# Performance work log

Measured on AMD Instinct MI355X. Metric: run time of the kernel, lower is better.

## Reference

```python
import jax, jax.numpy as jnp
from jax import lax
import numpy as np

B, T, N, F_IN, H, E, K = 8, 32, 500, 64, 128, 8000, 3
LN_EPS = 1e-5


def setup_inputs() -> dict:
    key = jax.random.key(0)
    ks = jax.random.split(key, 10)
    x = jax.random.normal(ks[0], (B, T, N, F_IN), dtype=jnp.float32)
    edge_index = jax.random.randint(ks[1], (2, E), 0, N, dtype=jnp.int64)
    edge_weight = jax.random.uniform(ks[2], (E,), dtype=jnp.float32)
    # GCNConv: linear (in->out) + bias
    W_gcn = jax.random.normal(ks[3], (F_IN, H), dtype=jnp.float32) / np.sqrt(F_IN)
    b_gcn = jnp.zeros((H,), dtype=jnp.float32)
    # Conv1d(H, H, K): weight (O, I, K)
    W_temp = jax.random.normal(ks[4], (H, H, K), dtype=jnp.float32) / np.sqrt(H * K)
    b_temp = jnp.zeros((H,), dtype=jnp.float32)
    # LayerNorm(H)
    ln_w = jnp.ones((H,), dtype=jnp.float32)
    ln_b = jnp.zeros((H,), dtype=jnp.float32)
    # residual Linear (in->out)
    W_res = jax.random.normal(ks[5], (F_IN, H), dtype=jnp.float32) / np.sqrt(F_IN)
    b_res = jnp.zeros((H,), dtype=jnp.float32)
    return {"x": x, "edge_index": edge_index, "edge_weight": edge_weight,
            "W_gcn": W_gcn, "b_gcn": b_gcn, "W_temp": W_temp, "b_temp": b_temp,
            "ln_w": ln_w, "ln_b": ln_b, "W_res": W_res, "b_res": b_res}


def reference(x, edge_index, edge_weight, W_gcn, b_gcn, W_temp, b_temp, ln_w, ln_b, W_res, b_res):
    Bv, Tv, Nv, Fv = x.shape
    Hv = W_gcn.shape[1]
    res = x @ W_res + b_res  # (B,T,N,H)

    # ---- spatial GCNConv on B*T replicated graphs (vectorized, no index offsetting) ----
    xf = x.reshape(Bv * Tv, Nv, Fv) @ W_gcn  # (BT,N,H)
    src, dst = edge_index[0], edge_index[1]
    loops = jnp.arange(Nv, dtype=edge_index.dtype)
    src2 = jnp.concatenate([src, loops])
    dst2 = jnp.concatenate([dst, loops])
    ew2 = jnp.concatenate([edge_weight, jnp.ones((Nv,), dtype=edge_weight.dtype)])
    deg = jax.ops.segment_sum(ew2, dst2, num_segments=Nv)
    dinv = jnp.where(deg > 0, deg ** -0.5, 0.0)
    norm = dinv[src2] * ew2 * dinv[dst2]  # (E+N,)
    msgs = xf[:, src2, :] * norm[None, :, None]  # (BT, E+N, H)
    agg = jax.vmap(lambda m: jax.ops.segment_sum(m, dst2, num_segments=Nv))(msgs)
    h = jax.nn.gelu(agg + b_gcn, approximate=False)  # (BT,N,H)

    # ---- temporal Conv1d over T ----
    h = h.reshape(Bv, Tv, Nv, Hv).transpose(0, 2, 3, 1).reshape(Bv * Nv, Hv, Tv)
    pad = K // 2
    h = lax.conv_general_dilated(h, W_temp, window_strides=(1,), padding=[(pad, pad)],
                                 dimension_numbers=("NCH", "OIH", "NCH"))
    h = jax.nn.gelu(h + b_temp[None, :, None], approximate=False)
    h = h.reshape(Bv, Nv, Hv, Tv).transpose(0, 3, 1, 2)  # (B,T,N,H)

    # ---- fused residual + LayerNorm over last dim ----
    y = h + res
    mu = jnp.mean(y, axis=-1, keepdims=True)
    var = jnp.mean((y - mu) ** 2, axis=-1, keepdims=True)
    return (y - mu) * lax.rsqrt(var + LN_EPS) * ln_w + ln_b
```

## Files before the change

kernel.cpp:

```cpp
#include <hip/hip_runtime.h>
#include <hip/hip_bf16.h>
#include <math.h>

#define Bv 8
#define Tv 32
#define Nv 500
#define Fin 64
#define Hv 128
#define Ev 8000
#define Kv 3
#define BT (Bv*Tv)
#define ROWS (BT*Nv)
#define TP (Tv+2)
#define KK (Kv*Hv)
#define LDSROW 136

typedef __attribute__((ext_vector_type(8))) short s8v;
typedef __attribute__((ext_vector_type(4))) float f4v;

__device__ __forceinline__ float gelu_exact(float v){
    return 0.5f*v*(1.0f + erff(v*0.70710678118654752440f));
}
__device__ __forceinline__ short f2bs(float f){
    union { __hip_bfloat16 h; short s; } u;
    u.h = __float2bfloat16(f);
    return u.s;
}
__device__ __forceinline__ float b2f(short s){
    union { unsigned int i; float f; } u;
    u.i = ((unsigned int)(unsigned short)s) << 16;
    return u.f;
}

__global__ void k_graph(const int* ei, const float* ew, float* deg, int* counts){
    int idx = blockIdx.x*256 + threadIdx.x;
    if (idx < Ev){
        int d = ei[Ev + idx];
        atomicAdd(&deg[d], ew[idx]);
        atomicAdd(&counts[d], 1);
    } else if (idx < Ev + Nv){
        atomicAdd(&deg[idx - Ev], 1.0f);
    }
}

__global__ void k_scan(const float* deg, const int* counts, float* dinv, int* offs, int* cursor){
    __shared__ int sa[512], sb[512];
    int tid = threadIdx.x;
    int c = (tid < Nv) ? counts[tid] : 0;
    if (tid < Nv){
        float d = deg[tid];
        dinv[tid] = (d > 0.f) ? rsqrtf(d) : 0.f;
    }
    sa[tid] = c; __syncthreads();
    int* s = sa; int* t = sb;
    for (int off = 1; off < 512; off <<= 1){
        int v = s[tid];
        if (tid >= off) v += s[tid - off];
        t[tid] = v; __syncthreads();
        int* tmp = s; s = t; t = tmp;
    }
    int excl = s[tid] - c;
    if (tid < Nv){ offs[tid] = excl; cursor[tid] = excl; }
    if (tid == 0) offs[Nv] = Ev;
}

__global__ void k_fill(const int* ei, const float* ew, const float* dinv,
                       int* cursor, int* csrc, float* cw){
    int e = blockIdx.x*256 + threadIdx.x;
    if (e >= Ev) return;
    int s = ei[e], d = ei[Ev + e];
    int pos = atomicAdd(&cursor[d], 1);
    csrc[pos] = s;
    cw[pos] = dinv[s]*ew[e]*dinv[d];
}

__global__ void k_wprep(const float* W, const float* Wg, const float* Wr,
                        short* W2, short* Wgt, short* Wrt){
    int idx = blockIdx.x*256 + threadIdx.x;
    if (idx < Hv*Hv*Kv){
        int o = idx/(Hv*Kv);
        int rem = idx - o*(Hv*Kv);
        int i = rem/Kv, k = rem - i*Kv;
        W2[o*KK + k*Hv + i] = f2bs(W[idx]);
    } else if (idx < Hv*Hv*Kv + Hv*64){
        int j = idx - Hv*Hv*Kv;
        int o = j >> 6, k = j & 63;
        Wgt[j] = f2bs(Wg[k*Hv + o]);
    } else if (idx < Hv*Hv*Kv + 2*Hv*64){
        int j = idx - Hv*Hv*Kv - Hv*64;
        int o = j >> 6, k = j & 63;
        Wrt[j] = f2bs(Wr[k*Hv + o]);
    }
}

__global__ __launch_bounds__(256) void k_xpose(const float* __restrict__ x,
        short* __restrict__ X2b, short* __restrict__ xb){
    int gid = blockIdx.x*256 + threadIdx.x;
    int row = gid >> 4, c4 = gid & 15;
    int bt = row / Nv;
    int n  = row - bt*Nv;
    float4 v = ((const float4*)x)[gid];
    short4 s;
    s.x = f2bs(v.x); s.y = f2bs(v.y); s.z = f2bs(v.z); s.w = f2bs(v.w);
    *(short4*)(xb + (size_t)row*64 + c4*4) = s;
    *(short4*)(X2b + (size_t)n*(BT*64) + bt*64 + c4*4) = s;
}

__global__ __launch_bounds__(256) void k_spmm(const short* __restrict__ X2b,
        const float* __restrict__ dinv, const int* __restrict__ offs,
        const int* __restrict__ csrc, const float* __restrict__ cw,
        short* __restrict__ AGG2){
    int bid = blockIdx.x;
    int ct = bid / Nv;
    int n  = bid - ct*Nv;
    int col = ct*2048 + threadIdx.x*8;
    float dv = dinv[n];
    float sw = dv*dv;
    float acc[8];
    s8v v = *(const s8v*)(X2b + (size_t)n*(BT*64) + col);
    #pragma unroll
    for (int q = 0; q < 8; ++q) acc[q] = sw * b2f(v[q]);
    int e0 = offs[n], e1 = offs[n+1];
    for (int e = e0; e < e1; ++e){
        int s = csrc[e]; float w = cw[e];
        s8v u = *(const s8v*)(X2b + (size_t)s*(BT*64) + col);
        #pragma unroll
        for (int q = 0; q < 8; ++q) acc[q] = fmaf(w, b2f(u[q]), acc[q]);
    }
    s8v r;
    #pragma unroll
    for (int q = 0; q < 8; ++q) r[q] = f2bs(acc[q]);
    *(s8v*)(AGG2 + (size_t)n*(BT*64) + col) = r;
}

__global__ __launch_bounds__(64) void k_gemm_gcn(const short* __restrict__ AGG2,
        const short* __restrict__ Wgt, const float* __restrict__ bg,
        short* __restrict__ hgp){
    __shared__ short ls[16*Hv];
    int lane = threadIdx.x;
    int laneo = lane & 15, quad = lane >> 4;
    int r0 = blockIdx.x * 16;
    const short* ap = AGG2 + (size_t)(r0 + laneo)*64 + quad*8;
    s8v a0 = *(const s8v*)ap;
    s8v a1 = *(const s8v*)(ap + 32);
    const short* wp = Wgt + laneo*64 + quad*8;
    f4v acc[8];
    #pragma unroll
    for (int nt = 0; nt < 8; ++nt){
        s8v b0 = *(const s8v*)(wp + nt*1024);
        s8v b1 = *(const s8v*)(wp + nt*1024 + 32);
        f4v z = {0.f,0.f,0.f,0.f};
        acc[nt] = __builtin_amdgcn_mfma_f32_16x16x32_bf16(a0, b0, z, 0,0,0);
        acc[nt] = __builtin_amdgcn_mfma_f32_16x16x32_bf16(a1, b1, acc[nt], 0,0,0);
    }
    #pragma unroll
    for (int nt = 0; nt < 8; ++nt){
        int o = nt*16 + laneo;
        float bb = bg[o];
        #pragma unroll
        for (int r = 0; r < 4; ++r){
            int row = quad*4 + r;
            ls[row*Hv + o] = f2bs(gelu_exact(acc[nt][r] + bb));
        }
    }
    __syncthreads();
    short* dst = hgp + (size_t)r0*Hv;
    #pragma unroll
    for (int it = 0; it < 4; ++it){
        int j = it*64 + lane;
        *(s8v*)(dst + j*8) = *(const s8v*)&ls[j*8];
    }
}

__global__ __launch_bounds__(64) void k_gemm_res(const short* __restrict__ xb,
        const short* __restrict__ Wrt, const float* __restrict__ br,
        float* __restrict__ out){
    __shared__ float ls[16*Hv];
    int lane = threadIdx.x;
    int laneo = lane & 15, quad = lane >> 4;
    int r0 = blockIdx.x * 16;
    const short* ap = xb + (size_t)(r0 + laneo)*64 + quad*8;
    s8v a0 = *(const s8v*)ap;
    s8v a1 = *(const s8v*)(ap + 32);
    const short* wp = Wrt + laneo*64 + quad*8;
    f4v acc[8];
    #pragma unroll
    for (int nt = 0; nt < 8; ++nt){
        s8v b0 = *(const s8v*)(wp + nt*1024);
        s8v b1 = *(const s8v*)(wp + nt*1024 + 32);
        f4v z = {0.f,0.f,0.f,0.f};
        acc[nt] = __builtin_amdgcn_mfma_f32_16x16x32_bf16(a0, b0, z, 0,0,0);
        acc[nt] = __builtin_amdgcn_mfma_f32_16x16x32_bf16(a1, b1, acc[nt], 0,0,0);
    }
    #pragma unroll
    for (int nt = 0; nt < 8; ++nt){
        int o = nt*16 + laneo;
        float bb = br[o];
        #pragma unroll
        for (int r = 0; r < 4; ++r){
            int row = quad*4 + r;
            ls[row*Hv + o] = acc[nt][r] + bb;
        }
    }
    __syncthreads();
    float* dst = out + (size_t)r0*Hv;
    #pragma unroll
    for (int it = 0; it < 8; ++it){
        int j = it*64 + lane;
        *(float4*)(dst + j*4) = *(const float4*)&ls[j*4];
    }
}

__global__ __launch_bounds__(256, 2) void k_conv(const short* __restrict__ hgp,
        const short* __restrict__ W2, const float* __restrict__ btm,
        const float* __restrict__ lw, const float* __restrict__ lb,
        float* __restrict__ out){
    __shared__ short hs[4*TP*LDSROW];
    __shared__ float red[Tv][4][2];
    int tid  = threadIdx.x;
    int w    = tid >> 6;
    int lane = tid & 63;
    int quad = lane >> 4;
    int laneo = lane & 15;
    int bid = blockIdx.x;
    int b  = bid / 125;
    int n0 = (bid - b*125) * 4;

    const short* hbase = hgp + ((size_t)n0*BT + b*Tv)*Hv;
    for (int j = tid; j < 4*Tv*16; j += 256){
        int node = j >> 9;
        int rem  = j & 511;
        s8v v = *(const s8v*)(hbase + (size_t)node*BT*Hv + rem*8);
        int tp = (rem >> 4) + 1, c8 = rem & 15;
        *(s8v*)&hs[node*(TP*LDSROW) + tp*LDSROW + c8*8] = v;
    }
    if (tid < 128){
        int node = tid >> 5, rem = tid & 31;
        int tp = (rem >> 4) * (TP-1), c8 = rem & 15;
        s8v z = {0,0,0,0,0,0,0,0};
        *(s8v*)&hs[node*(TP*LDSROW) + tp*LDSROW + c8*8] = z;
    }

    s8v breg[2][12];
    #pragma unroll
    for (int nt = 0; nt < 2; ++nt){
        int o = w*32 + nt*16 + laneo;
        const short* wp = W2 + o*KK + quad*8;
        #pragma unroll
        for (int s = 0; s < 12; ++s)
            breg[nt][s] = *(const s8v*)(wp + s*32);
    }
    float bb[2], lwv[2], lbv[2];
    #pragma unroll
    for (int nt = 0; nt < 2; ++nt){
        int o = w*32 + nt*16 + laneo;
        bb[nt] = btm[o]; lwv[nt] = lw[o]; lbv[nt] = lb[o];
    }
    __syncthreads();

    for (int g = 0; g < 4; ++g){
        int n = n0 + g;
        f4v acc[2][2];
        #pragma unroll
        for (int m = 0; m < 2; ++m)
            #pragma unroll
            for (int nt = 0; nt < 2; ++nt)
                acc[m][nt] = (f4v){0.f,0.f,0.f,0.f};
        #pragma unroll
        for (int m = 0; m < 2; ++m){
            #pragma unroll
            for (int s = 0; s < 12; ++s){
                int k  = s >> 2;
                int i0 = (s & 3) * 32;
                int tp = m*16 + laneo + k;
                s8v a = *(const s8v*)&hs[g*(TP*LDSROW) + tp*LDSROW + i0 + quad*8];
                acc[m][0] = __builtin_amdgcn_mfma_f32_16x16x32_bf16(a, breg[0][s], acc[m][0], 0,0,0);
                acc[m][1] = __builtin_amdgcn_mfma_f32_16x16x32_bf16(a, breg[1][s], acc[m][1], 0,0,0);
            }
        }
        size_t obase = ((size_t)b*Tv*Nv + n)*Hv;
        float yv[2][2][4];
        float srow[2][4], ssrow[2][4];
        #pragma unroll
        for (int m = 0; m < 2; ++m)
            #pragma unroll
            for (int r = 0; r < 4; ++r){ srow[m][r] = 0.f; ssrow[m][r] = 0.f; }
        #pragma unroll
        for (int m = 0; m < 2; ++m){
            #pragma unroll
            for (int nt = 0; nt < 2; ++nt){
                int o = w*32 + nt*16 + laneo;
                #pragma unroll
                for (int r = 0; r < 4; ++r){
                    int t = m*16 + quad*4 + r;
                    float gv = gelu_exact(acc[m][nt][r] + bb[nt]);
                    float y = gv + out[obase + (size_t)t*Nv*Hv + o];
                    yv[m][nt][r] = y;
                    srow[m][r] += y; ssrow[m][r] += y*y;
                }
            }
        }
        #pragma unroll
        for (int m = 0; m < 2; ++m)
            #pragma unroll
            for (int r = 0; r < 4; ++r){
                #pragma unroll
                for (int msk = 8; msk >= 1; msk >>= 1){
                    srow[m][r]  += __shfl_xor(srow[m][r],  msk, 64);
                    ssrow[m][r] += __shfl_xor(ssrow[m][r], msk, 64);
                }
            }
        if (laneo == 0){
            #pragma unroll
            for (int m = 0; m < 2; ++m)
                #pragma unroll
                for (int r = 0; r < 4; ++r){
                    int t = m*16 + quad*4 + r;
                    red[t][w][0] = srow[m][r];
                    red[t][w][1] = ssrow[m][r];
                }
        }
        __syncthreads();
        #pragma unroll
        for (int m = 0; m < 2; ++m){
            #pragma unroll
            for (int r = 0; r < 4; ++r){
                int t = m*16 + quad*4 + r;
                float s  = red[t][0][0] + red[t][1][0] + red[t][2][0] + red[t][3][0];
                float ss = red[t][0][1] + red[t][1][1] + red[t][2][1] + red[t][3][1];
                float mu = s * (1.f/128.f);
                float var = fmaxf(ss * (1.f/128.f) - mu*mu, 0.f);
                float rstd = rsqrtf(var + 1e-5f);
                #pragma unroll
                for (int nt = 0; nt < 2; ++nt){
                    int o = w*32 + nt*16 + laneo;
                    out[obase + (size_t)t*Nv*Hv + o] =
                        (yv[m][nt][r] - mu)*rstd*lwv[nt] + lbv[nt];
                }
            }
        }
        __syncthreads();
    }
}

extern "C" void kernel_launch(void* const* d_in, const int* in_sizes, int n_in,
                              void* d_out, int out_size, void* d_ws, size_t ws_size,
                              hipStream_t stream){
    const float* x   = (const float*)d_in[0];
    const int*   ei  = (const int*)d_in[1];
    const float* ew  = (const float*)d_in[2];
    const float* Wg  = (const float*)d_in[3];
    const float* bg  = (const float*)d_in[4];
    const float* Wtm = (const float*)d_in[5];
    const float* btm = (const float*)d_in[6];
    const float* lw  = (const float*)d_in[7];
    const float* lb  = (const float*)d_in[8];
    const float* Wr  = (const float*)d_in[9];
    const float* br  = (const float*)d_in[10];
    float* out = (float*)d_out;

    char* ws = (char*)d_ws;
    float* deg    = (float*)(ws + 0);
    int*   counts = (int*)  (ws + 2048);
    float* dinv   = (float*)(ws + 4096);
    int*   offs   = (int*)  (ws + 6144);
    int*   cursor = (int*)  (ws + 8192);
    int*   csrc   = (int*)  (ws + 10240);
    float* cwn    = (float*)(ws + 43008);
    short* W2     = (short*)(ws + 75776);
    short* Wgt    = (short*)(ws + 174080);
    short* Wrt    = (short*)(ws + 190464);
    short* X2b    = (short*)(ws + 206848);
    short* xb     = (short*)(ws + 16590848);
    short* AGG2   = (short*)(ws + 32974848);
    short* hgp    = (short*)(ws + 49358848);

    hipMemsetAsync(ws, 0, 4096, stream);

    k_graph   <<<(Ev+Nv+255)/256, 256, 0, stream>>>(ei, ew, deg, counts);
    k_scan    <<<1, 512, 0, stream>>>(deg, counts, dinv, offs, cursor);
    k_fill    <<<(Ev+255)/256, 256, 0, stream>>>(ei, ew, dinv, cursor, csrc, cwn);
    k_wprep   <<<256, 256, 0, stream>>>(Wtm, Wg, Wr, W2, Wgt, Wrt);
    k_xpose   <<<ROWS/16, 256, 0, stream>>>(x, X2b, xb);
    k_spmm    <<<8*Nv, 256, 0, stream>>>(X2b, dinv, offs, csrc, cwn, AGG2);
    k_gemm_gcn<<<ROWS/16, 64, 0, stream>>>(AGG2, Wgt, bg, hgp);
    k_gemm_res<<<ROWS/16, 64, 0, stream>>>(xb, Wrt, br, out);
    k_conv    <<<(Bv*Nv)/4, 256, 0, stream>>>(hgp, W2, btm, lw, lb, out);
}
```

Baseline: 246.9 us.

## Fuse GCN and residual GEMMs into conv/LayerNorm kernel and merge graph prep kernels

Folds the GCN linear+GELU GEMM and the residual linear GEMM into the temporal-conv kernel. The GCN output is written directly into LDS instead of going through a global intermediate, and the residual is computed in registers instead of being written to and re-read from the output buffer. The degree, scan and CSR-fill kernels are merged into one single-block kernel that uses shared-memory atomics, and weight prep is merged into the transpose kernel. The separate xb copy and the memset are dropped. This removes several launches and large global round trips, at the cost of more registers and MFMA work inside the conv kernel, plus a serial single-block prep and a changed LDS row padding.

```diff
diff --git a/kernel.cpp b/kernel.cpp
--- a/kernel.cpp
+++ b/kernel.cpp
@@ -13,7 +13,7 @@
 #define ROWS (BT*Nv)
 #define TP (Tv+2)
 #define KK (Kv*Hv)
-#define LDSROW 136
+#define LDSROW 144
 
 typedef __attribute__((ext_vector_type(8))) short s8v;
 typedef __attribute__((ext_vector_type(4))) float f4v;
@@ -32,78 +32,81 @@
     return u.f;
 }
 
-__global__ void k_graph(const int* ei, const float* ew, float* deg, int* counts){
-    int idx = blockIdx.x*256 + threadIdx.x;
-    if (idx < Ev){
-        int d = ei[Ev + idx];
-        atomicAdd(&deg[d], ew[idx]);
-        atomicAdd(&counts[d], 1);
-    } else if (idx < Ev + Nv){
-        atomicAdd(&deg[idx - Ev], 1.0f);
-    }
-}
-
-__global__ void k_scan(const float* deg, const int* counts, float* dinv, int* offs, int* cursor){
-    __shared__ int sa[512], sb[512];
+__global__ __launch_bounds__(1024) void k_prep(const int* __restrict__ ei,
+        const float* __restrict__ ew, float* __restrict__ dinv,
+        int* __restrict__ offs, int* __restrict__ csrc, float* __restrict__ cw){
+    __shared__ float sdeg[Nv];
+    __shared__ int   scnt[Nv];
+    __shared__ float sdv[Nv];
+    __shared__ int   scur[Nv];
+    __shared__ int   sa[512], sb[512];
     int tid = threadIdx.x;
-    int c = (tid < Nv) ? counts[tid] : 0;
+    if (tid < Nv){ sdeg[tid] = 1.0f; scnt[tid] = 0; }
+    __syncthreads();
+    for (int e = tid; e < Ev; e += 1024){
+        int d = ei[Ev + e];
+        atomicAdd(&sdeg[d], ew[e]);
+        atomicAdd(&scnt[d], 1);
+    }
+    __syncthreads();
+    int c = 0;
     if (tid < Nv){
-        float d = deg[tid];
-        dinv[tid] = (d > 0.f) ? rsqrtf(d) : 0.f;
-    }
-    sa[tid] = c; __syncthreads();
+        float d = sdeg[tid];
+        float v = (d > 0.f) ? rsqrtf(d) : 0.f;
+        sdv[tid] = v; dinv[tid] = v;
+    }
+    if (tid < 512){ c = (tid < Nv) ? scnt[tid] : 0; sa[tid] = c; }
+    __syncthreads();
     int* s = sa; int* t = sb;
     for (int off = 1; off < 512; off <<= 1){
-        int v = s[tid];
-        if (tid >= off) v += s[tid - off];
-        t[tid] = v; __syncthreads();
+        int v = 0;
+        if (tid < 512){ v = s[tid]; if (tid >= off) v += s[tid - off]; }
+        if (tid < 512) t[tid] = v;
+        __syncthreads();
         int* tmp = s; s = t; t = tmp;
     }
-    int excl = s[tid] - c;
-    if (tid < Nv){ offs[tid] = excl; cursor[tid] = excl; }
+    if (tid < Nv){ int excl = s[tid] - c; offs[tid] = excl; scur[tid] = excl; }
     if (tid == 0) offs[Nv] = Ev;
-}
-
-__global__ void k_fill(const int* ei, const float* ew, const float* dinv,
-                       int* cursor, int* csrc, float* cw){
-    int e = blockIdx.x*256 + threadIdx.x;
-    if (e >= Ev) return;
-    int s = ei[e], d = ei[Ev + e];
-    int pos = atomicAdd(&cursor[d], 1);
-    csrc[pos] = s;
-    cw[pos] = dinv[s]*ew[e]*dinv[d];
-}
-
-__global__ void k_wprep(const float* W, const float* Wg, const float* Wr,
-                        short* W2, short* Wgt, short* Wrt){
-    int idx = blockIdx.x*256 + threadIdx.x;
-    if (idx < Hv*Hv*Kv){
-        int o = idx/(Hv*Kv);
-        int rem = idx - o*(Hv*Kv);
-        int i = rem/Kv, k = rem - i*Kv;
-        W2[o*KK + k*Hv + i] = f2bs(W[idx]);
-    } else if (idx < Hv*Hv*Kv + Hv*64){
-        int j = idx - Hv*Hv*Kv;
-        int o = j >> 6, k = j & 63;
-        Wgt[j] = f2bs(Wg[k*Hv + o]);
-    } else if (idx < Hv*Hv*Kv + 2*Hv*64){
-        int j = idx - Hv*Hv*Kv - Hv*64;
-        int o = j >> 6, k = j & 63;
-        Wrt[j] = f2bs(Wr[k*Hv + o]);
+    __syncthreads();
+    for (int e = tid; e < Ev; e += 1024){
+        int sn = ei[e], d = ei[Ev + e];
+        int pos = atomicAdd(&scur[d], 1);
+        csrc[pos] = sn;
+        cw[pos] = sdv[sn]*ew[e]*sdv[d];
     }
 }
 
 __global__ __launch_bounds__(256) void k_xpose(const float* __restrict__ x,
-        short* __restrict__ X2b, short* __restrict__ xb){
-    int gid = blockIdx.x*256 + threadIdx.x;
-    int row = gid >> 4, c4 = gid & 15;
-    int bt = row / Nv;
-    int n  = row - bt*Nv;
-    float4 v = ((const float4*)x)[gid];
-    short4 s;
-    s.x = f2bs(v.x); s.y = f2bs(v.y); s.z = f2bs(v.z); s.w = f2bs(v.w);
-    *(short4*)(xb + (size_t)row*64 + c4*4) = s;
-    *(short4*)(X2b + (size_t)n*(BT*64) + bt*64 + c4*4) = s;
+        short* __restrict__ X2b, const float* __restrict__ W,
+        const float* __restrict__ Wg, const float* __restrict__ Wr,
+        short* __restrict__ W2, short* __restrict__ Wgt, short* __restrict__ Wrt){
+    int bid = blockIdx.x;
+    if (bid < ROWS/16){
+        int gid = bid*256 + threadIdx.x;
+        int row = gid >> 4, c4 = gid & 15;
+        int bt = row / Nv;
+        int n  = row - bt*Nv;
+        float4 v = ((const float4*)x)[gid];
+        short4 sv;
+        sv.x = f2bs(v.x); sv.y = f2bs(v.y); sv.z = f2bs(v.z); sv.w = f2bs(v.w);
+        *(short4*)(X2b + (size_t)n*(BT*64) + bt*64 + c4*4) = sv;
+    } else {
+        int idx = (bid - ROWS/16)*256 + threadIdx.x;
+        if (idx < Hv*Hv*Kv){
+            int o = idx/(Hv*Kv);
+            int rem = idx - o*(Hv*Kv);
+            int i = rem/Kv, k = rem - i*Kv;
+            W2[o*KK + k*Hv + i] = f2bs(W[idx]);
+        } else if (idx < Hv*Hv*Kv + Hv*64){
+            int j = idx - Hv*Hv*Kv;
+            int o = j >> 6, k = j & 63;
+            Wgt[j] = f2bs(Wg[k*Hv + o]);
+        } else if (idx < Hv*Hv*Kv + 2*Hv*64){
+            int j = idx - Hv*Hv*Kv - Hv*64;
+            int o = j >> 6, k = j & 63;
+            Wrt[j] = f2bs(Wr[k*Hv + o]);
+        }
+    }
 }
 
 __global__ __launch_bounds__(256) void k_spmm(const short* __restrict__ X2b,
@@ -133,88 +136,13 @@
     *(s8v*)(AGG2 + (size_t)n*(BT*64) + col) = r;
 }
 
-__global__ __launch_bounds__(64) void k_gemm_gcn(const short* __restrict__ AGG2,
-        const short* __restrict__ Wgt, const float* __restrict__ bg,
-        short* __restrict__ hgp){
-    __shared__ short ls[16*Hv];
-    int lane = threadIdx.x;
-    int laneo = lane & 15, quad = lane >> 4;
-    int r0 = blockIdx.x * 16;
-    const short* ap = AGG2 + (size_t)(r0 + laneo)*64 + quad*8;
-    s8v a0 = *(const s8v*)ap;
-    s8v a1 = *(const s8v*)(ap + 32);
-    const short* wp = Wgt + laneo*64 + quad*8;
-    f4v acc[8];
-    #pragma unroll
-    for (int nt = 0; nt < 8; ++nt){
-        s8v b0 = *(const s8v*)(wp + nt*1024);
-        s8v b1 = *(const s8v*)(wp + nt*1024 + 32);
-        f4v z = {0.f,0.f,0.f,0.f};
-        acc[nt] = __builtin_amdgcn_mfma_f32_16x16x32_bf16(a0, b0, z, 0,0,0);
-        acc[nt] = __builtin_amdgcn_mfma_f32_16x16x32_bf16(a1, b1, acc[nt], 0,0,0);
-    }
-    #pragma unroll
-    for (int nt = 0; nt < 8; ++nt){
-        int o = nt*16 + laneo;
-        float bb = bg[o];
-        #pragma unroll
-        for (int r = 0; r < 4; ++r){
-            int row = quad*4 + r;
-            ls[row*Hv + o] = f2bs(gelu_exact(acc[nt][r] + bb));
-        }
-    }
-    __syncthreads();
-    short* dst = hgp + (size_t)r0*Hv;
-    #pragma unroll
-    for (int it = 0; it < 4; ++it){
-        int j = it*64 + lane;
-        *(s8v*)(dst + j*8) = *(const s8v*)&ls[j*8];
-    }
-}
-
-__global__ __launch_bounds__(64) void k_gemm_res(const short* __restrict__ xb,
-        const short* __restrict__ Wrt, const float* __restrict__ br,
-        float* __restrict__ out){
-    __shared__ float ls[16*Hv];
-    int lane = threadIdx.x;
-    int laneo = lane & 15, quad = lane >> 4;
-    int r0 = blockIdx.x * 16;
-    const short* ap = xb + (size_t)(r0 + laneo)*64 + quad*8;
-    s8v a0 = *(const s8v*)ap;
-    s8v a1 = *(const s8v*)(ap + 32);
-    const short* wp = Wrt + laneo*64 + quad*8;
-    f4v acc[8];
-    #pragma unroll
-    for (int nt = 0; nt < 8; ++nt){
-        s8v b0 = *(const s8v*)(wp + nt*1024);
-        s8v b1 = *(const s8v*)(wp + nt*1024 + 32);
-        f4v z = {0.f,0.f,0.f,0.f};
-        acc[nt] = __builtin_amdgcn_mfma_f32_16x16x32_bf16(a0, b0, z, 0,0,0);
-        acc[nt] = __builtin_amdgcn_mfma_f32_16x16x32_bf16(a1, b1, acc[nt], 0,0,0);
-    }
-    #pragma unroll
-    for (int nt = 0; nt < 8; ++nt){
-        int o = nt*16 + laneo;
-        float bb = br[o];
-        #pragma unroll
-        for (int r = 0; r < 4; ++r){
-            int row = quad*4 + r;
-            ls[row*Hv + o] = acc[nt][r] + bb;
-        }
-    }
-    __syncthreads();
-    float* dst = out + (size_t)r0*Hv;
-    #pragma unroll
-    for (int it = 0; it < 8; ++it){
-        int j = it*64 + lane;
-        *(float4*)(dst + j*4) = *(const float4*)&ls[j*4];
-    }
-}
-
-__global__ __launch_bounds__(256, 2) void k_conv(const short* __restrict__ hgp,
-        const short* __restrict__ W2, const float* __restrict__ btm,
-        const float* __restrict__ lw, const float* __restrict__ lb,
-        float* __restrict__ out){
+__global__ __launch_bounds__(256, 2) void k_mega(
+        const short* __restrict__ AGG2, const short* __restrict__ X2b,
+        const short* __restrict__ W2, const short* __restrict__ Wgt,
+        const short* __restrict__ Wrt,
+        const float* __restrict__ bg, const float* __restrict__ btm,
+        const float* __restrict__ br, const float* __restrict__ lw,
+        const float* __restrict__ lb, float* __restrict__ out){
     __shared__ short hs[4*TP*LDSROW];
     __shared__ float red[Tv][4][2];
     int tid  = threadIdx.x;
@@ -225,36 +153,65 @@
     int bid = blockIdx.x;
     int b  = bid / 125;
     int n0 = (bid - b*125) * 4;
-
-    const short* hbase = hgp + ((size_t)n0*BT + b*Tv)*Hv;
-    for (int j = tid; j < 4*Tv*16; j += 256){
-        int node = j >> 9;
-        int rem  = j & 511;
-        s8v v = *(const s8v*)(hbase + (size_t)node*BT*Hv + rem*8);
-        int tp = (rem >> 4) + 1, c8 = rem & 15;
-        *(s8v*)&hs[node*(TP*LDSROW) + tp*LDSROW + c8*8] = v;
-    }
+    int o_base = w*32;
+
+    float bgv[2], bbv[2], brv[2], lwv[2], lbv[2];
+    #pragma unroll
+    for (int nt = 0; nt < 2; ++nt){
+        int o = o_base + nt*16 + laneo;
+        bgv[nt] = bg[o]; bbv[nt] = btm[o]; brv[nt] = br[o];
+        lwv[nt] = lw[o]; lbv[nt] = lb[o];
+    }
+
+    s8v bwg[2][2];
+    #pragma unroll
+    for (int nt = 0; nt < 2; ++nt){
+        const short* wp = Wgt + (o_base + nt*16 + laneo)*64 + quad*8;
+        bwg[nt][0] = *(const s8v*)wp;
+        bwg[nt][1] = *(const s8v*)(wp + 32);
+    }
+
     if (tid < 128){
         int node = tid >> 5, rem = tid & 31;
-        int tp = (rem >> 4) * (TP-1), c8 = rem & 15;
+        int tp = (rem >> 4)*(TP-1), c8 = rem & 15;
         s8v z = {0,0,0,0,0,0,0,0};
         *(s8v*)&hs[node*(TP*LDSROW) + tp*LDSROW + c8*8] = z;
     }
 
-    s8v breg[2][12];
+    for (int g = 0; g < 4; ++g){
+        int n = n0 + g;
+        const short* ap = AGG2 + ((size_t)n*BT + b*Tv)*64;
+        #pragma unroll
+        for (int m = 0; m < 2; ++m){
+            const short* arp = ap + (m*16 + laneo)*64 + quad*8;
+            s8v a0 = *(const s8v*)arp;
+            s8v a1 = *(const s8v*)(arp + 32);
+            f4v h0 = {0.f,0.f,0.f,0.f}, h1 = {0.f,0.f,0.f,0.f};
+            h0 = __builtin_amdgcn_mfma_f32_16x16x32_bf16(a0, bwg[0][0], h0, 0,0,0);
+            h0 = __builtin_amdgcn_mfma_f32_16x16x32_bf16(a1, bwg[0][1], h0, 0,0,0);
+            h1 = __builtin_amdgcn_mfma_f32_16x16x32_bf16(a0, bwg[1][0], h1, 0,0,0);
+            h1 = __builtin_amdgcn_mfma_f32_16x16x32_bf16(a1, bwg[1][1], h1, 0,0,0);
+            #pragma unroll
+            for (int r = 0; r < 4; ++r){
+                int tp = m*16 + quad*4 + r + 1;
+                short* hrow = &hs[g*(TP*LDSROW) + tp*LDSROW];
+                hrow[o_base + laneo]      = f2bs(gelu_exact(h0[r] + bgv[0]));
+                hrow[o_base + 16 + laneo] = f2bs(gelu_exact(h1[r] + bgv[1]));
+            }
+        }
+    }
+
+    s8v breg[2][12], bwr[2][2];
     #pragma unroll
     for (int nt = 0; nt < 2; ++nt){
-        int o = w*32 + nt*16 + laneo;
+        int o = o_base + nt*16 + laneo;
         const short* wp = W2 + o*KK + quad*8;
         #pragma unroll
         for (int s = 0; s < 12; ++s)
             breg[nt][s] = *(const s8v*)(wp + s*32);
-    }
-    float bb[2], lwv[2], lbv[2];
-    #pragma unroll
-    for (int nt = 0; nt < 2; ++nt){
-        int o = w*32 + nt*16 + laneo;
-        bb[nt] = btm[o]; lwv[nt] = lw[o]; lbv[nt] = lb[o];
+        const short* wr = Wrt + o*64 + quad*8;
+        bwr[nt][0] = *(const s8v*)wr;
+        bwr[nt][1] = *(const s8v*)(wr + 32);
     }
     __syncthreads();
 
@@ -278,6 +235,23 @@
                 acc[m][1] = __builtin_amdgcn_mfma_f32_16x16x32_bf16(a, breg[1][s], acc[m][1], 0,0,0);
             }
         }
+        f4v racc[2][2];
+        #pragma unroll
+        for (int m = 0; m < 2; ++m)
+            #pragma unroll
+            for (int nt = 0; nt < 2; ++nt)
+                racc[m][nt] = (f4v){0.f,0.f,0.f,0.f};
+        const short* xp = X2b + ((size_t)n*BT + b*Tv)*64;
+        #pragma unroll
+        for (int m = 0; m < 2; ++m){
+            const short* xrp = xp + (m*16 + laneo)*64 + quad*8;
+            s8v a0 = *(const s8v*)xrp;
+            s8v a1 = *(const s8v*)(xrp + 32);
+            racc[m][0] = __builtin_amdgcn_mfma_f32_16x16x32_bf16(a0, bwr[0][0], racc[m][0], 0,0,0);
+            racc[m][0] = __builtin_amdgcn_mfma_f32_16x16x32_bf16(a1, bwr[0][1], racc[m][0], 0,0,0);
+            racc[m][1] = __builtin_amdgcn_mfma_f32_16x16x32_bf16(a0, bwr[1][0], racc[m][1], 0,0,0);
+            racc[m][1] = __builtin_amdgcn_mfma_f32_16x16x32_bf16(a1, bwr[1][1], racc[m][1], 0,0,0);
+        }
         size_t obase = ((size_t)b*Tv*Nv + n)*Hv;
         float yv[2][2][4];
         float srow[2][4], ssrow[2][4];
@@ -289,12 +263,10 @@
         for (int m = 0; m < 2; ++m){
             #pragma unroll
             for (int nt = 0; nt < 2; ++nt){
-                int o = w*32 + nt*16 + laneo;
                 #pragma unroll
                 for (int r = 0; r < 4; ++r){
-                    int t = m*16 + quad*4 + r;
-                    float gv = gelu_exact(acc[m][nt][r] + bb[nt]);
-                    float y = gv + out[obase + (size_t)t*Nv*Hv + o];
+                    float gv = gelu_exact(acc[m][nt][r] + bbv[nt]);
+                    float y = gv + racc[m][nt][r] + brv[nt];
                     yv[m][nt][r] = y;
                     srow[m][r] += y; ssrow[m][r] += y*y;
                 }
@@ -333,7 +305,7 @@
                 float rstd = rsqrtf(var + 1e-5f);
                 #pragma unroll
                 for (int nt = 0; nt < 2; ++nt){
-                    int o = w*32 + nt*16 + laneo;
+                    int o = o_base + nt*16 + laneo;
                     out[obase + (size_t)t*Nv*Hv + o] =
                         (yv[m][nt][r] - mu)*rstd*lwv[nt] + lbv[nt];
                 }
@@ -360,30 +332,19 @@
     float* out = (float*)d_out;
 
     char* ws = (char*)d_ws;
-    float* deg    = (float*)(ws + 0);
-    int*   counts = (int*)  (ws + 2048);
-    float* dinv   = (float*)(ws + 4096);
-    int*   offs   = (int*)  (ws + 6144);
-    int*   cursor = (int*)  (ws + 8192);
-    int*   csrc   = (int*)  (ws + 10240);
-    float* cwn    = (float*)(ws + 43008);
-    short* W2     = (short*)(ws + 75776);
-    short* Wgt    = (short*)(ws + 174080);
-    short* Wrt    = (short*)(ws + 190464);
-    short* X2b    = (short*)(ws + 206848);
-    short* xb     = (short*)(ws + 16590848);
-    short* AGG2   = (short*)(ws + 32974848);
-    short* hgp    = (short*)(ws + 49358848);
-
-    hipMemsetAsync(ws, 0, 4096, stream);
-
-    k_graph   <<<(Ev+Nv+255)/256, 256, 0, stream>>>(ei, ew, deg, counts);
-    k_scan    <<<1, 512, 0, stream>>>(deg, counts, dinv, offs, cursor);
-    k_fill    <<<(Ev+255)/256, 256, 0, stream>>>(ei, ew, dinv, cursor, csrc, cwn);
-    k_wprep   <<<256, 256, 0, stream>>>(Wtm, Wg, Wr, W2, Wgt, Wrt);
-    k_xpose   <<<ROWS/16, 256, 0, stream>>>(x, X2b, xb);
-    k_spmm    <<<8*Nv, 256, 0, stream>>>(X2b, dinv, offs, csrc, cwn, AGG2);
-    k_gemm_gcn<<<ROWS/16, 64, 0, stream>>>(AGG2, Wgt, bg, hgp);
-    k_gemm_res<<<ROWS/16, 64, 0, stream>>>(xb, Wrt, br, out);
-    k_conv    <<<(Bv*Nv)/4, 256, 0, stream>>>(hgp, W2, btm, lw, lb, out);
-}
+    float* dinv = (float*)(ws + 0);
+    int*   offs = (int*)  (ws + 4096);
+    int*   csrc = (int*)  (ws + 8192);
+    float* cwn  = (float*)(ws + 40960);
+    short* W2   = (short*)(ws + 73728);
+    short* Wgt  = (short*)(ws + 172032);
+    short* Wrt  = (short*)(ws + 188416);
+    short* X2b  = (short*)(ws + 204800);
+    short* AGG2 = (short*)(ws + 16588800);
+
+    k_prep <<<1, 1024, 0, stream>>>(ei, ew, dinv, offs, csrc, cwn);
+    k_xpose<<<ROWS/16 + 256, 256, 0, stream>>>(x, X2b, Wtm, Wg, Wr, W2, Wgt, Wrt);
+    k_spmm <<<8*Nv, 256, 0, stream>>>(X2b, dinv, offs, csrc, cwn, AGG2);
+    k_mega <<<(Bv*Nv)/4, 256, 0, stream>>>(AGG2, X2b, W2, Wgt, Wrt,
+                                           bg, btm, br, lw, lb, out);
+}
```

After: 218.7 us. -11.4%, faster.
